# Kernel optimization log

Measured on AMD Instinct MI355X. Metric: run time of the kernel, lower is better.

The kernel has to match this reference:

```python
import jax, jax.numpy as jnp
import numpy as np

EMBED_DIM = 1024
NUM_HEADS = 16
HEAD_DIM = EMBED_DIM // NUM_HEADS


def setup_inputs() -> dict:
    key = jax.random.key(0)
    ks = jax.random.split(key, 6)
    s = 1.0 / np.sqrt(EMBED_DIM)
    return {
        "x": jax.random.normal(ks[0], (4, 2048, EMBED_DIM), dtype=jnp.float32),
        "Wq": jax.random.uniform(ks[1], (EMBED_DIM, EMBED_DIM), jnp.float32, -s, s),
        "Wk": jax.random.uniform(ks[2], (EMBED_DIM, EMBED_DIM), jnp.float32, -s, s),
        "Wv": jax.random.uniform(ks[3], (EMBED_DIM, EMBED_DIM), jnp.float32, -s, s),
        "Wo": jax.random.uniform(ks[4], (EMBED_DIM, EMBED_DIM), jnp.float32, -s, s),
        "bo": jax.random.uniform(ks[5], (EMBED_DIM,), jnp.float32, -s, s),
    }


def reference(x, Wq, Wk, Wv, Wo, bo):
    B, S, E = x.shape
    H, D = NUM_HEADS, HEAD_DIM
    # torch Linear: x @ W.T ; reshape to [B, H, S, D]
    q = (x @ Wq.T).reshape(B, S, H, D).transpose(0, 2, 1, 3)
    k = (x @ Wk.T).reshape(B, S, H, D).transpose(0, 2, 1, 3)
    v = (x @ Wv.T).reshape(B, S, H, D).transpose(0, 2, 1, 3)
    scores = jnp.einsum("bhqd,bhkd->bhqk", q, k) / jnp.sqrt(jnp.float32(D))
    attn = jax.nn.softmax(scores, axis=-1)  # dropout is identity in eval mode
    out = jnp.einsum("bhqk,bhkd->bhqd", attn, v)
    out = out.transpose(0, 2, 1, 3).reshape(B, S, E)
    return out @ Wo.T + bo
```

## Files before the change

kernel.cpp:

```cpp
#include <hip/hip_runtime.h>
#include <hip/hip_bf16.h>
#include <math.h>

#define B_ 4
#define S_ 2048
#define E_ 1024
#define H_ 16
#define D_ 64
#define M_ (B_*S_)
#define NKV 32

typedef __attribute__((ext_vector_type(8))) short short8;
typedef __attribute__((ext_vector_type(4))) short short4_t;
typedef __attribute__((ext_vector_type(4))) float f32x4;
typedef __attribute__((ext_vector_type(16))) float f32x16;

static __device__ __forceinline__ short f2bf(float f){
  union { float f; unsigned u; } v; v.f = f;
  unsigned u = v.u + 0x7FFFu + ((v.u >> 16) & 1u);
  return (short)(u >> 16);
}

__global__ void cast_all(const float* __restrict__ x,
    const float* __restrict__ wq, const float* __restrict__ wk,
    const float* __restrict__ wv, const float* __restrict__ wo,
    short8* __restrict__ xb, short8* __restrict__ wqb, short8* __restrict__ wkb,
    short8* __restrict__ wvb, short8* __restrict__ wob){
  int bid = blockIdx.x;
  const float* src; short8* dst; int i;
  if (bid < 4096) { src = x; dst = xb; i = bid*256 + threadIdx.x; }
  else {
    int k = (bid - 4096) >> 9;
    i = ((bid - 4096) & 511)*256 + threadIdx.x;
    src = k==0 ? wq : k==1 ? wk : k==2 ? wv : wo;
    dst = k==0 ? wqb : k==1 ? wkb : k==2 ? wvb : wob;
  }
  const float4* s4 = (const float4*)src;
  float4 a = s4[2*i], b = s4[2*i+1];
  short8 o;
  o[0]=f2bf(a.x); o[1]=f2bf(a.y); o[2]=f2bf(a.z); o[3]=f2bf(a.w);
  o[4]=f2bf(b.x); o[5]=f2bf(b.y); o[6]=f2bf(b.z); o[7]=f2bf(b.w);
  dst[i]=o;
}

#define GLOAD16(g, l) __builtin_amdgcn_global_load_lds( \
    (const __attribute__((address_space(1))) void*)(g), \
    (__attribute__((address_space(3))) void*)(l), 16, 0, 0)

#define BARF __builtin_amdgcn_s_barrier(); \
             asm volatile("" ::: "memory"); \
             __builtin_amdgcn_sched_barrier(0);

__global__ __launch_bounds__(512,1) void gemm_qkv(const short* __restrict__ A,
      const short* __restrict__ Wf, short* __restrict__ Qo, short* __restrict__ Ko,
      short* __restrict__ Vto, float u)
{
  extern __shared__ char LDSc[];
  const int tid = threadIdx.x;
  const int w = tid >> 6, lane = tid & 63;
  const int l15 = lane & 15, l4 = lane >> 4;
  const int rx = l15 & 7;
  const int wm = w >> 2, wn = w & 3;
  const int m0 = blockIdx.x * 256;
  const int n0 = blockIdx.y * 192;

  const int lanerow = lane >> 3;
  const int lchunk8 = ((lane & 7) ^ lanerow) * 8;
  const short* Aq = A  + (size_t)(m0 + w*8 + lanerow)*1024 + lchunk8;
  const short* Bq = Wf + (size_t)(n0 + w*8 + lanerow)*1024 + lchunk8;

  #define STA(kt,i) GLOAD16(Aq + (size_t)((i)*64)*1024 + (kt)*64, \
      LDSc + ((kt)&1)*57344 + (i)*8192 + w*1024);
  #define STB(kt,i) GLOAD16(Bq + (size_t)((i)*64)*1024 + (kt)*64, \
      LDSc + ((kt)&1)*57344 + 32768 + (i)*8192 + w*1024);

  f32x4 acc[8][3] = {};

  STA(0,0) STA(0,1) STA(0,2) STA(0,3)
  STB(0,0) STB(0,1) STB(0,2)
  asm volatile("s_waitcnt vmcnt(0)" ::: "memory");
  BARF

  #define RDA(QM) \
    _Pragma("unroll") for (int i_ = 0; i_ < 4; ++i_) \
    _Pragma("unroll") for (int ks_ = 0; ks_ < 2; ++ks_) \
      af_[i_][ks_] = *(const short8*)(Ab + (wm*128 + (QM)*64 + i_*16 + l15)*128 + (((ks_*4 + l4) ^ rx)*16));
  #define RDB \
    _Pragma("unroll") for (int j_ = 0; j_ < 3; ++j_) \
    _Pragma("unroll") for (int ks_ = 0; ks_ < 2; ++ks_) \
      bf_[j_][ks_] = *(const short8*)(Bb + (wn*48 + j_*16 + l15)*128 + (((ks_*4 + l4) ^ rx)*16));
  #define MF(QM) \
    __builtin_amdgcn_s_setprio(1); \
    _Pragma("unroll") for (int i_ = 0; i_ < 4; ++i_) \
    _Pragma("unroll") for (int j_ = 0; j_ < 3; ++j_) \
    _Pragma("unroll") for (int ks_ = 0; ks_ < 2; ++ks_) \
      acc[(QM)*4+i_][j_] = __builtin_amdgcn_mfma_f32_16x16x32_bf16( \
          af_[i_][ks_], bf_[j_][ks_], acc[(QM)*4+i_][j_], 0,0,0); \
    __builtin_amdgcn_s_setprio(0);

  for (int k = 0; k < 16; ++k) {
    const char* Ab = LDSc + (k & 1)*57344;
    const char* Bb = Ab + 32768;
    const bool st = (k < 15);
    short8 af_[4][2], bf_[3][2];
    RDA(0)
    RDB
    if (st) { STA(k+1,0) STA(k+1,1) STA(k+1,2) STA(k+1,3) }
    BARF
    MF(0)
    BARF
    RDA(1)
    if (st) { STB(k+1,0) STB(k+1,1) STB(k+1,2) }
    BARF
    MF(1)
    asm volatile("s_waitcnt vmcnt(0)" ::: "memory");
    BARF
  }
  #undef RDA
  #undef RDB
  #undef MF
  #undef STA
  #undef STB

  #pragma unroll
  for (int i = 0; i < 8; ++i) {
    int row = m0 + wm*128 + i*16 + 4*l4;
    int b = row >> 11;
    int s0 = row & 2047;
    #pragma unroll
    for (int j = 0; j < 3; ++j) {
      int col = n0 + wn*48 + j*16 + l15;
      int sel = col >> 10;
      int colm = col & 1023;
      int h = colm >> 6, d = colm & 63;
      if (sel == 2) {
        short4_t pk;
        pk[0]=f2bf(acc[i][j][0]); pk[1]=f2bf(acc[i][j][1]);
        pk[2]=f2bf(acc[i][j][2]); pk[3]=f2bf(acc[i][j][3]);
        *(short4_t*)(Vto + (((size_t)(b*H_ + h))*D_ + d)*S_ + s0) = pk;
      } else {
        short* O = sel ? Ko : Qo;
        float sc = sel ? 1.0f : u;
        #pragma unroll
        for (int r = 0; r < 4; ++r) {
          int s = (s0 + r) & 2047;
          O[(((size_t)(b*H_ + h))*S_ + s)*D_ + d] = f2bf(acc[i][j][r]*sc);
        }
      }
    }
  }
}

__global__ __launch_bounds__(512,1) void gemm_out(const short* __restrict__ A,
      const short* __restrict__ W, float* __restrict__ out,
      const float* __restrict__ bias)
{
  extern __shared__ char LDSc[];
  const int tid = threadIdx.x;
  const int w = tid >> 6, lane = tid & 63;
  const int l15 = lane & 15, l4 = lane >> 4;
  const int rx = l15 & 7;
  const int wm = w >> 2, wn = w & 3;
  const int m0 = blockIdx.x * 256;
  const int n0 = blockIdx.y * 128;

  const int lanerow = lane >> 3;
  const int lchunk8 = ((lane & 7) ^ lanerow) * 8;
  const short* Aq = A + (size_t)(m0 + w*8 + lanerow)*1024 + lchunk8;
  const short* Bq = W + (size_t)(n0 + w*8 + lanerow)*1024 + lchunk8;

  #define STA(kt,i) GLOAD16(Aq + (size_t)((i)*64)*1024 + (kt)*64, \
      LDSc + ((kt)&1)*49152 + (i)*8192 + w*1024);
  #define STB(kt,i) GLOAD16(Bq + (size_t)((i)*64)*1024 + (kt)*64, \
      LDSc + ((kt)&1)*49152 + 32768 + (i)*8192 + w*1024);

  f32x4 acc[8][2] = {};

  STA(0,0) STA(0,1) STA(0,2) STA(0,3)
  STB(0,0) STB(0,1)
  asm volatile("s_waitcnt vmcnt(0)" ::: "memory");
  BARF

  #define RDA(QM) \
    _Pragma("unroll") for (int i_ = 0; i_ < 4; ++i_) \
    _Pragma("unroll") for (int ks_ = 0; ks_ < 2; ++ks_) \
      af_[i_][ks_] = *(const short8*)(Ab + (wm*128 + (QM)*64 + i_*16 + l15)*128 + (((ks_*4 + l4) ^ rx)*16));
  #define RDB \
    _Pragma("unroll") for (int j_ = 0; j_ < 2; ++j_) \
    _Pragma("unroll") for (int ks_ = 0; ks_ < 2; ++ks_) \
      bf_[j_][ks_] = *(const short8*)(Bb + (wn*32 + j_*16 + l15)*128 + (((ks_*4 + l4) ^ rx)*16));
  #define MF(QM) \
    __builtin_amdgcn_s_setprio(1); \
    _Pragma("unroll") for (int i_ = 0; i_ < 4; ++i_) \
    _Pragma("unroll") for (int j_ = 0; j_ < 2; ++j_) \
    _Pragma("unroll") for (int ks_ = 0; ks_ < 2; ++ks_) \
      acc[(QM)*4+i_][j_] = __builtin_amdgcn_mfma_f32_16x16x32_bf16( \
          af_[i_][ks_], bf_[j_][ks_], acc[(QM)*4+i_][j_], 0,0,0); \
    __builtin_amdgcn_s_setprio(0);

  for (int k = 0; k < 16; ++k) {
    const char* Ab = LDSc + (k & 1)*49152;
    const char* Bb = Ab + 32768;
    const bool st = (k < 15);
    short8 af_[4][2], bf_[2][2];
    RDA(0)
    RDB
    if (st) { STA(k+1,0) STA(k+1,1) STA(k+1,2) STA(k+1,3) }
    BARF
    MF(0)
    BARF
    RDA(1)
    if (st) { STB(k+1,0) STB(k+1,1) }
    BARF
    MF(1)
    asm volatile("s_waitcnt vmcnt(0)" ::: "memory");
    BARF
  }
  #undef RDA
  #undef RDB
  #undef MF
  #undef STA
  #undef STB

  #pragma unroll
  for (int i = 0; i < 8; ++i) {
    int row = m0 + wm*128 + i*16 + 4*l4;
    #pragma unroll
    for (int j = 0; j < 2; ++j) {
      int col = n0 + wn*32 + j*16 + l15;
      float bz = bias[col];
      #pragma unroll
      for (int r = 0; r < 4; ++r)
        out[(size_t)(row + r)*1024 + col] = acc[i][j][r] + bz;
    }
  }
}

static __device__ __forceinline__ unsigned cvtpk(float lo, float hi){
  unsigned d; asm("v_cvt_pk_bf16_f32 %0, %1, %2" : "=v"(d) : "v"(lo), "v"(hi)); return d;
}
static __device__ __forceinline__ void plswap(unsigned &a, unsigned &b){
  asm("v_permlane32_swap_b32 %0, %1" : "+v"(a), "+v"(b));
}
template<int BASE>
static __device__ __forceinline__ short8 pfrag(const f32x16 &s){
  unsigned w01 = cvtpk(s[BASE+0], s[BASE+1]);
  unsigned w23 = cvtpk(s[BASE+2], s[BASE+3]);
  unsigned w45 = cvtpk(s[BASE+4], s[BASE+5]);
  unsigned w67 = cvtpk(s[BASE+6], s[BASE+7]);
  plswap(w01, w45);
  plswap(w23, w67);
  union { unsigned u[4]; short8 s8; } r;
  r.u[0]=w01; r.u[1]=w23; r.u[2]=w45; r.u[3]=w67;
  return r.s8;
}

__global__ __launch_bounds__(256,4) void attn_kernel(const short* __restrict__ Qb,
    const short* __restrict__ Kb, const short* __restrict__ Vtb, short* __restrict__ Ob)
{
  __shared__ short KL[2][64*64];
  __shared__ short VL[2][64*64];
  const int tid = threadIdx.x, w = tid >> 6, lane = tid & 63;
  const int l31 = lane & 31, hi = lane >> 5;
  const int rx7 = l31 & 7;

  const int linear = blockIdx.x;
  const int swz = (linear & 7)*128 + (linear >> 3);
  const int bh = swz >> 4;
  const int b = bh >> 4, h = bh & 15;
  const int q0 = (swz & 15) * 128;

  const short* Qg = Qb + ((size_t)bh*S_ + q0)*D_;
  const short* Kg = Kb + (size_t)bh*S_*D_;
  const short* Vg = Vtb + (size_t)bh*D_*S_;

  const int srow = tid >> 3;
  const int scol = ((tid & 7) ^ (srow & 7)) * 8;

  #define STAGE(t, bi) { \
    GLOAD16(Kg + (size_t)((t)*64 +      srow)*D_ + scol, (char*)KL[bi] + w*1024); \
    GLOAD16(Kg + (size_t)((t)*64 + 32 + srow)*D_ + scol, (char*)KL[bi] + 4096 + w*1024); \
    GLOAD16(Vg + (size_t)(     srow)*S_ + (t)*64 + scol, (char*)VL[bi] + w*1024); \
    GLOAD16(Vg + (size_t)(32 + srow)*S_ + (t)*64 + scol, (char*)VL[bi] + 4096 + w*1024); }

  STAGE(0, 0)

  const int qrow = w*32 + l31;
  short8 qf[4];
  #pragma unroll
  for (int t = 0; t < 4; ++t)
    qf[t] = *(const short8*)(Qg + (size_t)qrow*D_ + (2*t + hi)*8);

  short8 ones;
  #pragma unroll
  for (int t = 0; t < 8; ++t) ones[t] = (short)0x3F80;

  f32x16 oacc[2] = {};
  f32x16 lacc = {};

  for (int kv = 0; kv < NKV; ++kv) {
    const int cur = kv & 1;
    if (kv < NKV-1) {
      STAGE(kv+1, cur^1)
      asm volatile("s_waitcnt vmcnt(4)" ::: "memory");
    } else {
      asm volatile("s_waitcnt vmcnt(0)" ::: "memory");
    }
    __builtin_amdgcn_s_barrier();
    asm volatile("" ::: "memory");
    __builtin_amdgcn_sched_barrier(0);

    f32x16 st[2] = {};
    __builtin_amdgcn_s_setprio(1);
    #pragma unroll
    for (int t = 0; t < 4; ++t) {
      int co = ((2*t + hi) ^ rx7)*16;
      short8 ka0 = *(const short8*)((char*)KL[cur] + l31*128 + co);
      short8 ka1 = *(const short8*)((char*)KL[cur] + (32 + l31)*128 + co);
      st[0] = __builtin_amdgcn_mfma_f32_32x32x16_bf16(ka0, qf[t], st[0], 0,0,0);
      st[1] = __builtin_amdgcn_mfma_f32_32x32x16_bf16(ka1, qf[t], st[1], 0,0,0);
    }
    __builtin_amdgcn_s_setprio(0);

    #pragma unroll
    for (int r = 0; r < 16; ++r) st[0][r] = __builtin_amdgcn_exp2f(st[0][r]);
    #pragma unroll
    for (int r = 0; r < 16; ++r) st[1][r] = __builtin_amdgcn_exp2f(st[1][r]);

    short8 pf[4];
    pf[0] = pfrag<0>(st[0]);
    pf[1] = pfrag<8>(st[0]);
    pf[2] = pfrag<0>(st[1]);
    pf[3] = pfrag<8>(st[1]);

    __builtin_amdgcn_s_setprio(1);
    #pragma unroll
    for (int t = 0; t < 4; ++t) {
      int co = ((2*t + hi) ^ rx7)*16;
      short8 va0 = *(const short8*)((char*)VL[cur] + l31*128 + co);
      short8 va1 = *(const short8*)((char*)VL[cur] + (32 + l31)*128 + co);
      oacc[0] = __builtin_amdgcn_mfma_f32_32x32x16_bf16(va0, pf[t], oacc[0], 0,0,0);
      oacc[1] = __builtin_amdgcn_mfma_f32_32x32x16_bf16(va1, pf[t], oacc[1], 0,0,0);
      lacc = __builtin_amdgcn_mfma_f32_32x32x16_bf16(ones, pf[t], lacc, 0,0,0);
    }
    __builtin_amdgcn_s_setprio(0);
    __builtin_amdgcn_sched_barrier(0);
    asm volatile("" ::: "memory");
    __builtin_amdgcn_s_barrier();
    asm volatile("" ::: "memory");
  }
  #undef STAGE

  float inv = 1.f / lacc[0];
  int s = q0 + qrow;
  short* orow = Ob + ((size_t)(b*S_ + s))*E_ + h*64;
  #pragma unroll
  for (int r = 0; r < 16; r += 2) {
    int d0 = (r & 3) + 8*(r >> 2) + 4*hi;
    unsigned pa = (unsigned short)f2bf(oacc[0][r]*inv) |
                  ((unsigned)(unsigned short)f2bf(oacc[0][r+1]*inv) << 16);
    unsigned pb = (unsigned short)f2bf(oacc[1][r]*inv) |
                  ((unsigned)(unsigned short)f2bf(oacc[1][r+1]*inv) << 16);
    *(unsigned*)(orow + d0) = pa;
    *(unsigned*)(orow + 32 + d0) = pb;
  }
}

extern "C" void kernel_launch(void* const* d_in, const int* in_sizes, int n_in,
                              void* d_out, int out_size, void* d_ws, size_t ws_size,
                              hipStream_t stream) {
  const float* x  = (const float*)d_in[0];
  const float* Wq = (const float*)d_in[1];
  const float* Wk = (const float*)d_in[2];
  const float* Wv = (const float*)d_in[3];
  const float* Wo = (const float*)d_in[4];
  const float* bo = (const float*)d_in[5];

  char* ws = (char*)d_ws;
  short* xb  = (short*)(ws);
  short* Wqb = (short*)(ws + (16u<<20));
  short* Wkb = (short*)(ws + (18u<<20));
  short* Wvb = (short*)(ws + (20u<<20));
  short* Wob = (short*)(ws + (22u<<20));
  short* Qb  = (short*)(ws + (24u<<20));
  short* Kb  = (short*)(ws + (40u<<20));
  short* Vtb = (short*)(ws + (56u<<20));
  short* Ab  = (short*)(ws + (72u<<20));

  cast_all<<<4096 + 4*512, 256, 0, stream>>>(x, Wq, Wk, Wv, Wo,
      (short8*)xb, (short8*)Wqb, (short8*)Wkb, (short8*)Wvb, (short8*)Wob);

  const float u = 0.18033688011112042f;
  gemm_qkv<<<dim3(32, 16), 512, 114688, stream>>>(xb, Wqb, Qb, Kb, Vtb, u);

  attn_kernel<<<1024, 256, 0, stream>>>(Qb, Kb, Vtb, Ab);

  gemm_out<<<dim3(32, 8), 512, 98304, stream>>>(Ab, Wob, (float*)d_out, bo);
}
```

Baseline: 175.9 us.

## Shrink QKV GEMM tiles to 256x128 with BK=32 for two blocks per CU

The QKV GEMM tile goes from 256x192 with K-step 64 to 256x128 with K-step 32. That cuts LDS use to 48KB and enables launch_bounds(512,2), so two blocks can be resident per CU, and the grid grows to 32x24. The LDS swizzle and load mapping are reworked for 64-byte rows, and the epilogue hoists the Q/K/V selection out of the loops since each block now maps to a single projection. Attention launch bounds are also raised to 5 waves, which adds register pressure and risks spills. The smaller K step doubles the barrier and loop overhead per FLOP.

```diff
diff --git a/kernel.cpp b/kernel.cpp
--- a/kernel.cpp
+++ b/kernel.cpp
@@ -51,7 +51,7 @@
              asm volatile("" ::: "memory"); \
              __builtin_amdgcn_sched_barrier(0);
 
-__global__ __launch_bounds__(512,1) void gemm_qkv(const short* __restrict__ A,
+__global__ __launch_bounds__(512,2) void gemm_qkv(const short* __restrict__ A,
       const short* __restrict__ Wf, short* __restrict__ Qo, short* __restrict__ Ko,
       short* __restrict__ Vto, float u)
 {
@@ -59,58 +59,54 @@
   const int tid = threadIdx.x;
   const int w = tid >> 6, lane = tid & 63;
   const int l15 = lane & 15, l4 = lane >> 4;
-  const int rx = l15 & 7;
+  const int rxr = (l15 >> 1) & 3;
   const int wm = w >> 2, wn = w & 3;
   const int m0 = blockIdx.x * 256;
-  const int n0 = blockIdx.y * 192;
-
-  const int lanerow = lane >> 3;
-  const int lchunk8 = ((lane & 7) ^ lanerow) * 8;
-  const short* Aq = A  + (size_t)(m0 + w*8 + lanerow)*1024 + lchunk8;
-  const short* Bq = Wf + (size_t)(n0 + w*8 + lanerow)*1024 + lchunk8;
-
-  #define STA(kt,i) GLOAD16(Aq + (size_t)((i)*64)*1024 + (kt)*64, \
-      LDSc + ((kt)&1)*57344 + (i)*8192 + w*1024);
-  #define STB(kt,i) GLOAD16(Bq + (size_t)((i)*64)*1024 + (kt)*64, \
-      LDSc + ((kt)&1)*57344 + 32768 + (i)*8192 + w*1024);
-
-  f32x4 acc[8][3] = {};
-
-  STA(0,0) STA(0,1) STA(0,2) STA(0,3)
-  STB(0,0) STB(0,1) STB(0,2)
+  const int n0 = blockIdx.y * 128;
+
+  const int lrow = lane >> 2;
+  const int lch  = lane & 3;
+  const int sch  = (lch ^ ((lrow >> 1) & 3)) * 8;
+  const short* Aq = A  + (size_t)(m0 + w*16 + lrow)*1024 + sch;
+  const short* Bq = Wf + (size_t)(n0 + w*16 + lrow)*1024 + sch;
+
+  #define STA(kt,i) GLOAD16(Aq + (size_t)((i)*128)*1024 + (kt)*32, \
+      LDSc + ((kt)&1)*24576 + (i)*8192 + w*1024);
+  #define STB(kt) GLOAD16(Bq + (size_t)(kt)*32, \
+      LDSc + ((kt)&1)*24576 + 16384 + w*1024);
+
+  f32x4 acc[8][2] = {};
+
+  STA(0,0) STA(0,1) STB(0)
   asm volatile("s_waitcnt vmcnt(0)" ::: "memory");
   BARF
 
   #define RDA(QM) \
     _Pragma("unroll") for (int i_ = 0; i_ < 4; ++i_) \
-    _Pragma("unroll") for (int ks_ = 0; ks_ < 2; ++ks_) \
-      af_[i_][ks_] = *(const short8*)(Ab + (wm*128 + (QM)*64 + i_*16 + l15)*128 + (((ks_*4 + l4) ^ rx)*16));
+      af_[i_] = *(const short8*)(Ab + (wm*128 + (QM)*64 + i_*16 + l15)*64 + ((l4 ^ rxr)*16));
   #define RDB \
-    _Pragma("unroll") for (int j_ = 0; j_ < 3; ++j_) \
-    _Pragma("unroll") for (int ks_ = 0; ks_ < 2; ++ks_) \
-      bf_[j_][ks_] = *(const short8*)(Bb + (wn*48 + j_*16 + l15)*128 + (((ks_*4 + l4) ^ rx)*16));
+    _Pragma("unroll") for (int j_ = 0; j_ < 2; ++j_) \
+      bf_[j_] = *(const short8*)(Ab + 16384 + (wn*32 + j_*16 + l15)*64 + ((l4 ^ rxr)*16));
   #define MF(QM) \
     __builtin_amdgcn_s_setprio(1); \
     _Pragma("unroll") for (int i_ = 0; i_ < 4; ++i_) \
-    _Pragma("unroll") for (int j_ = 0; j_ < 3; ++j_) \
-    _Pragma("unroll") for (int ks_ = 0; ks_ < 2; ++ks_) \
+    _Pragma("unroll") for (int j_ = 0; j_ < 2; ++j_) \
       acc[(QM)*4+i_][j_] = __builtin_amdgcn_mfma_f32_16x16x32_bf16( \
-          af_[i_][ks_], bf_[j_][ks_], acc[(QM)*4+i_][j_], 0,0,0); \
+          af_[i_], bf_[j_], acc[(QM)*4+i_][j_], 0,0,0); \
     __builtin_amdgcn_s_setprio(0);
 
-  for (int k = 0; k < 16; ++k) {
-    const char* Ab = LDSc + (k & 1)*57344;
-    const char* Bb = Ab + 32768;
-    const bool st = (k < 15);
-    short8 af_[4][2], bf_[3][2];
+  for (int k = 0; k < 32; ++k) {
+    const char* Ab = LDSc + (k & 1)*24576;
+    const bool st = (k < 31);
+    short8 af_[4], bf_[2];
     RDA(0)
     RDB
-    if (st) { STA(k+1,0) STA(k+1,1) STA(k+1,2) STA(k+1,3) }
+    if (st) { STA(k+1,0) STA(k+1,1) }
     BARF
     MF(0)
     BARF
     RDA(1)
-    if (st) { STB(k+1,0) STB(k+1,1) STB(k+1,2) }
+    if (st) { STB(k+1) }
     BARF
     MF(1)
     asm volatile("s_waitcnt vmcnt(0)" ::: "memory");
@@ -122,28 +118,38 @@
   #undef STA
   #undef STB
 
-  #pragma unroll
-  for (int i = 0; i < 8; ++i) {
-    int row = m0 + wm*128 + i*16 + 4*l4;
-    int b = row >> 11;
-    int s0 = row & 2047;
-    #pragma unroll
-    for (int j = 0; j < 3; ++j) {
-      int col = n0 + wn*48 + j*16 + l15;
-      int sel = col >> 10;
-      int colm = col & 1023;
-      int h = colm >> 6, d = colm & 63;
-      if (sel == 2) {
+  const int sel = n0 >> 10;
+  const int nc0 = n0 & 1023;
+  if (sel == 2) {
+    #pragma unroll
+    for (int i = 0; i < 8; ++i) {
+      int row = m0 + wm*128 + i*16 + 4*l4;
+      int b = row >> 11;
+      int s0 = row & 2047;
+      #pragma unroll
+      for (int j = 0; j < 2; ++j) {
+        int col = nc0 + wn*32 + j*16 + l15;
+        int h = col >> 6, d = col & 63;
         short4_t pk;
         pk[0]=f2bf(acc[i][j][0]); pk[1]=f2bf(acc[i][j][1]);
         pk[2]=f2bf(acc[i][j][2]); pk[3]=f2bf(acc[i][j][3]);
         *(short4_t*)(Vto + (((size_t)(b*H_ + h))*D_ + d)*S_ + s0) = pk;
-      } else {
-        short* O = sel ? Ko : Qo;
-        float sc = sel ? 1.0f : u;
+      }
+    }
+  } else {
+    short* O = sel ? Ko : Qo;
+    float sc = sel ? 1.0f : u;
+    #pragma unroll
+    for (int i = 0; i < 8; ++i) {
+      int row = m0 + wm*128 + i*16 + 4*l4;
+      int b = row >> 11;
+      #pragma unroll
+      for (int j = 0; j < 2; ++j) {
+        int col = nc0 + wn*32 + j*16 + l15;
+        int h = col >> 6, d = col & 63;
         #pragma unroll
         for (int r = 0; r < 4; ++r) {
-          int s = (s0 + r) & 2047;
+          int s = (row + r) & 2047;
           O[(((size_t)(b*H_ + h))*S_ + s)*D_ + d] = f2bf(acc[i][j][r]*sc);
         }
       }
@@ -255,7 +261,7 @@
   return r.s8;
 }
 
-__global__ __launch_bounds__(256,4) void attn_kernel(const short* __restrict__ Qb,
+__global__ __launch_bounds__(256,5) void attn_kernel(const short* __restrict__ Qb,
     const short* __restrict__ Kb, const short* __restrict__ Vtb, short* __restrict__ Ob)
 {
   __shared__ short KL[2][64*64];
@@ -391,7 +397,7 @@
       (short8*)xb, (short8*)Wqb, (short8*)Wkb, (short8*)Wvb, (short8*)Wob);
 
   const float u = 0.18033688011112042f;
-  gemm_qkv<<<dim3(32, 16), 512, 114688, stream>>>(xb, Wqb, Qb, Kb, Vtb, u);
+  gemm_qkv<<<dim3(32, 24), 512, 49152, stream>>>(xb, Wqb, Qb, Kb, Vtb, u);
 
   attn_kernel<<<1024, 256, 0, stream>>>(Qb, Kb, Vtb, Ab);
 
```

Result: slower. 533.9 us (+203.5%).

## Switch projection GEMMs from 16x16x32 to 32x32x16 MFMA with new wave tiling

Applied to the files above, without the earlier changes.

Both the QKV and output projection GEMMs now use the 32x32x16 bf16 MFMA instead of 16x16x32. The wave layout changes from 2x4 to 4x2, so each wave owns a 64-row by 96- or 64-column tile, and the LDS fragment reads and epilogue indexing are rewritten to match. Larger MFMA tiles mean fewer LDS fragment loads per FLOP and fewer instruction issues. The cost is higher register pressure and a different LDS bank access pattern under the existing XOR swizzle.

```diff
diff --git a/kernel.cpp b/kernel.cpp
--- a/kernel.cpp
+++ b/kernel.cpp
@@ -58,9 +58,9 @@
   extern __shared__ char LDSc[];
   const int tid = threadIdx.x;
   const int w = tid >> 6, lane = tid & 63;
-  const int l15 = lane & 15, l4 = lane >> 4;
-  const int rx = l15 & 7;
-  const int wm = w >> 2, wn = w & 3;
+  const int l31 = lane & 31, hi = lane >> 5;
+  const int rx7 = l31 & 7;
+  const int wm = w >> 1, wn = w & 1;
   const int m0 = blockIdx.x * 256;
   const int n0 = blockIdx.y * 192;
 
@@ -74,35 +74,33 @@
   #define STB(kt,i) GLOAD16(Bq + (size_t)((i)*64)*1024 + (kt)*64, \
       LDSc + ((kt)&1)*57344 + 32768 + (i)*8192 + w*1024);
 
-  f32x4 acc[8][3] = {};
+  f32x16 acc[2][3] = {};
 
   STA(0,0) STA(0,1) STA(0,2) STA(0,3)
   STB(0,0) STB(0,1) STB(0,2)
   asm volatile("s_waitcnt vmcnt(0)" ::: "memory");
   BARF
 
-  #define RDA(QM) \
-    _Pragma("unroll") for (int i_ = 0; i_ < 4; ++i_) \
-    _Pragma("unroll") for (int ks_ = 0; ks_ < 2; ++ks_) \
-      af_[i_][ks_] = *(const short8*)(Ab + (wm*128 + (QM)*64 + i_*16 + l15)*128 + (((ks_*4 + l4) ^ rx)*16));
+  #define RDA(MT) \
+    _Pragma("unroll") for (int ks_ = 0; ks_ < 4; ++ks_) \
+      af_[ks_] = *(const short8*)(Ab + (wm*64 + (MT)*32 + l31)*128 + (((ks_*2 + hi) ^ rx7)*16));
   #define RDB \
-    _Pragma("unroll") for (int j_ = 0; j_ < 3; ++j_) \
-    _Pragma("unroll") for (int ks_ = 0; ks_ < 2; ++ks_) \
-      bf_[j_][ks_] = *(const short8*)(Bb + (wn*48 + j_*16 + l15)*128 + (((ks_*4 + l4) ^ rx)*16));
-  #define MF(QM) \
+    _Pragma("unroll") for (int nt_ = 0; nt_ < 3; ++nt_) \
+    _Pragma("unroll") for (int ks_ = 0; ks_ < 4; ++ks_) \
+      bf_[nt_][ks_] = *(const short8*)(Bb + (wn*96 + nt_*32 + l31)*128 + (((ks_*2 + hi) ^ rx7)*16));
+  #define MF(MT) \
     __builtin_amdgcn_s_setprio(1); \
-    _Pragma("unroll") for (int i_ = 0; i_ < 4; ++i_) \
-    _Pragma("unroll") for (int j_ = 0; j_ < 3; ++j_) \
-    _Pragma("unroll") for (int ks_ = 0; ks_ < 2; ++ks_) \
-      acc[(QM)*4+i_][j_] = __builtin_amdgcn_mfma_f32_16x16x32_bf16( \
-          af_[i_][ks_], bf_[j_][ks_], acc[(QM)*4+i_][j_], 0,0,0); \
+    _Pragma("unroll") for (int nt_ = 0; nt_ < 3; ++nt_) \
+    _Pragma("unroll") for (int ks_ = 0; ks_ < 4; ++ks_) \
+      acc[MT][nt_] = __builtin_amdgcn_mfma_f32_32x32x16_bf16( \
+          af_[ks_], bf_[nt_][ks_], acc[MT][nt_], 0,0,0); \
     __builtin_amdgcn_s_setprio(0);
 
   for (int k = 0; k < 16; ++k) {
     const char* Ab = LDSc + (k & 1)*57344;
     const char* Bb = Ab + 32768;
     const bool st = (k < 15);
-    short8 af_[4][2], bf_[3][2];
+    short8 af_[4], bf_[3][4];
     RDA(0)
     RDB
     if (st) { STA(k+1,0) STA(k+1,1) STA(k+1,2) STA(k+1,3) }
@@ -123,28 +121,35 @@
   #undef STB
 
   #pragma unroll
-  for (int i = 0; i < 8; ++i) {
-    int row = m0 + wm*128 + i*16 + 4*l4;
-    int b = row >> 11;
-    int s0 = row & 2047;
-    #pragma unroll
-    for (int j = 0; j < 3; ++j) {
-      int col = n0 + wn*48 + j*16 + l15;
+  for (int mt = 0; mt < 2; ++mt) {
+    #pragma unroll
+    for (int nt = 0; nt < 3; ++nt) {
+      int col = n0 + wn*96 + nt*32 + l31;
       int sel = col >> 10;
       int colm = col & 1023;
       int h = colm >> 6, d = colm & 63;
       if (sel == 2) {
-        short4_t pk;
-        pk[0]=f2bf(acc[i][j][0]); pk[1]=f2bf(acc[i][j][1]);
-        pk[2]=f2bf(acc[i][j][2]); pk[3]=f2bf(acc[i][j][3]);
-        *(short4_t*)(Vto + (((size_t)(b*H_ + h))*D_ + d)*S_ + s0) = pk;
+        #pragma unroll
+        for (int rq = 0; rq < 4; ++rq) {
+          int row = m0 + wm*64 + mt*32 + 8*rq + 4*hi;
+          int b = row >> 11;
+          int s0 = row & 2047;
+          short4_t pk;
+          pk[0]=f2bf(acc[mt][nt][rq*4+0]); pk[1]=f2bf(acc[mt][nt][rq*4+1]);
+          pk[2]=f2bf(acc[mt][nt][rq*4+2]); pk[3]=f2bf(acc[mt][nt][rq*4+3]);
+          *(short4_t*)(Vto + (((size_t)(b*H_ + h))*D_ + d)*S_ + s0) = pk;
+        }
       } else {
         short* O = sel ? Ko : Qo;
         float sc = sel ? 1.0f : u;
         #pragma unroll
-        for (int r = 0; r < 4; ++r) {
-          int s = (s0 + r) & 2047;
-          O[(((size_t)(b*H_ + h))*S_ + s)*D_ + d] = f2bf(acc[i][j][r]*sc);
+        for (int rq = 0; rq < 4; ++rq) {
+          int row = m0 + wm*64 + mt*32 + 8*rq + 4*hi;
+          int b = row >> 11;
+          int s0 = row & 2047;
+          #pragma unroll
+          for (int r2 = 0; r2 < 4; ++r2)
+            O[(((size_t)(b*H_ + h))*S_ + s0 + r2)*D_ + d] = f2bf(acc[mt][nt][rq*4+r2]*sc);
         }
       }
     }
@@ -158,9 +163,9 @@
   extern __shared__ char LDSc[];
   const int tid = threadIdx.x;
   const int w = tid >> 6, lane = tid & 63;
-  const int l15 = lane & 15, l4 = lane >> 4;
-  const int rx = l15 & 7;
-  const int wm = w >> 2, wn = w & 3;
+  const int l31 = lane & 31, hi = lane >> 5;
+  const int rx7 = l31 & 7;
+  const int wm = w >> 1, wn = w & 1;
   const int m0 = blockIdx.x * 256;
   const int n0 = blockIdx.y * 128;
 
@@ -174,35 +179,33 @@
   #define STB(kt,i) GLOAD16(Bq + (size_t)((i)*64)*1024 + (kt)*64, \
       LDSc + ((kt)&1)*49152 + 32768 + (i)*8192 + w*1024);
 
-  f32x4 acc[8][2] = {};
+  f32x16 acc[2][2] = {};
 
   STA(0,0) STA(0,1) STA(0,2) STA(0,3)
   STB(0,0) STB(0,1)
   asm volatile("s_waitcnt vmcnt(0)" ::: "memory");
   BARF
 
-  #define RDA(QM) \
-    _Pragma("unroll") for (int i_ = 0; i_ < 4; ++i_) \
-    _Pragma("unroll") for (int ks_ = 0; ks_ < 2; ++ks_) \
-      af_[i_][ks_] = *(const short8*)(Ab + (wm*128 + (QM)*64 + i_*16 + l15)*128 + (((ks_*4 + l4) ^ rx)*16));
+  #define RDA(MT) \
+    _Pragma("unroll") for (int ks_ = 0; ks_ < 4; ++ks_) \
+      af_[ks_] = *(const short8*)(Ab + (wm*64 + (MT)*32 + l31)*128 + (((ks_*2 + hi) ^ rx7)*16));
   #define RDB \
-    _Pragma("unroll") for (int j_ = 0; j_ < 2; ++j_) \
-    _Pragma("unroll") for (int ks_ = 0; ks_ < 2; ++ks_) \
-      bf_[j_][ks_] = *(const short8*)(Bb + (wn*32 + j_*16 + l15)*128 + (((ks_*4 + l4) ^ rx)*16));
-  #define MF(QM) \
+    _Pragma("unroll") for (int nt_ = 0; nt_ < 2; ++nt_) \
+    _Pragma("unroll") for (int ks_ = 0; ks_ < 4; ++ks_) \
+      bf_[nt_][ks_] = *(const short8*)(Bb + (wn*64 + nt_*32 + l31)*128 + (((ks_*2 + hi) ^ rx7)*16));
+  #define MF(MT) \
     __builtin_amdgcn_s_setprio(1); \
-    _Pragma("unroll") for (int i_ = 0; i_ < 4; ++i_) \
-    _Pragma("unroll") for (int j_ = 0; j_ < 2; ++j_) \
-    _Pragma("unroll") for (int ks_ = 0; ks_ < 2; ++ks_) \
-      acc[(QM)*4+i_][j_] = __builtin_amdgcn_mfma_f32_16x16x32_bf16( \
-          af_[i_][ks_], bf_[j_][ks_], acc[(QM)*4+i_][j_], 0,0,0); \
+    _Pragma("unroll") for (int nt_ = 0; nt_ < 2; ++nt_) \
+    _Pragma("unroll") for (int ks_ = 0; ks_ < 4; ++ks_) \
+      acc[MT][nt_] = __builtin_amdgcn_mfma_f32_32x32x16_bf16( \
+          af_[ks_], bf_[nt_][ks_], acc[MT][nt_], 0,0,0); \
     __builtin_amdgcn_s_setprio(0);
 
   for (int k = 0; k < 16; ++k) {
     const char* Ab = LDSc + (k & 1)*49152;
     const char* Bb = Ab + 32768;
     const bool st = (k < 15);
-    short8 af_[4][2], bf_[2][2];
+    short8 af_[4], bf_[2][4];
     RDA(0)
     RDB
     if (st) { STA(k+1,0) STA(k+1,1) STA(k+1,2) STA(k+1,3) }
@@ -223,15 +226,18 @@
   #undef STB
 
   #pragma unroll
-  for (int i = 0; i < 8; ++i) {
-    int row = m0 + wm*128 + i*16 + 4*l4;
-    #pragma unroll
-    for (int j = 0; j < 2; ++j) {
-      int col = n0 + wn*32 + j*16 + l15;
+  for (int mt = 0; mt < 2; ++mt) {
+    #pragma unroll
+    for (int nt = 0; nt < 2; ++nt) {
+      int col = n0 + wn*64 + nt*32 + l31;
       float bz = bias[col];
       #pragma unroll
-      for (int r = 0; r < 4; ++r)
-        out[(size_t)(row + r)*1024 + col] = acc[i][j][r] + bz;
+      for (int rq = 0; rq < 4; ++rq) {
+        int row = m0 + wm*64 + mt*32 + 8*rq + 4*hi;
+        #pragma unroll
+        for (int r2 = 0; r2 < 4; ++r2)
+          out[(size_t)(row + r2)*1024 + col] = acc[mt][nt][rq*4+r2] + bz;
+      }
     }
   }
 }
```

Result: slower. 183.4 us (+4.3%).
